# Kernel tuning notes

Hardware: AMD Instinct MI355X
Metric: run time of the kernel (lower is better)

## Reference

```python
import jax, jax.numpy as jnp
import numpy as np

B, T = 256, 2048
K_LABELS = 50
K2 = K_LABELS + 2  # includes START (K) and STOP (K+1) tags
NEG_INF = -10000.0


def setup_inputs() -> dict:
    key = jax.random.key(0)
    k1, k2, k3, k4 = jax.random.split(key, 4)
    emissions = jax.random.normal(k1, (B, T, K2), dtype=jnp.float32)
    transitions = jax.random.normal(k2, (K2, K2), dtype=jnp.float32)
    lengths = jax.random.randint(k3, (B,), 1, T + 1, dtype=jnp.int64)
    labels = jax.random.randint(k4, (B, T), 0, K_LABELS, dtype=jnp.int64)
    return {"emissions": emissions, "transitions": transitions,
            "lengths": lengths, "labels": labels}


def _forward_algo(emissions, transitions, lengths):
    b, t, k2 = emissions.shape
    start_tag, stop_tag = k2 - 2, k2 - 1
    init = jnp.full((k2,), NEG_INF, emissions.dtype).at[start_tag].set(0.0)
    alpha0 = jnp.broadcast_to(init, (b, k2))  # [B, K2]

    def step(alpha, emit):
        # tag_var[b, next, prev] = emit[b, next] + trans[next, prev] + alpha[b, prev]
        tag_var = emit[:, :, None] + transitions[None, :, :] + alpha[:, None, :]
        new_alpha = jax.nn.logsumexp(tag_var, axis=2)  # [B, K2]
        return new_alpha, new_alpha

    _, alphas = jax.lax.scan(step, alpha0, jnp.swapaxes(emissions, 0, 1))
    all_alphas = jnp.concatenate([alpha0[None], alphas], axis=0)  # [T+1, B, K2]
    fv = all_alphas[lengths, jnp.arange(b)]  # alpha at each sequence's final step
    terminal = fv + transitions[stop_tag][None, :]
    return jax.nn.logsumexp(terminal, axis=1)  # [B]


def _score_label(emissions, transitions, lengths, labels):
    b, t, k2 = emissions.shape
    start_tag, stop_tag = k2 - 2, k2 - 1
    start_col = jnp.full((b, 1), start_tag, labels.dtype)
    stop_col = jnp.full((b, 1), stop_tag, labels.dtype)
    pad_start = jnp.concatenate([start_col, labels], axis=1)  # [B, T+1]
    pad_stop = jnp.concatenate([labels, stop_col], axis=1)    # [B, T+1]
    pos = jnp.arange(t + 1)
    pad_stop = jnp.where(pos[None, :] >= lengths[:, None], stop_tag, pad_stop)
    # transition score over positions 0..length (inclusive)
    trans_mask = pos[None, :] <= lengths[:, None]
    trans_sc = jnp.where(trans_mask, transitions[pad_stop, pad_start], 0.0).sum(axis=1)
    # emission score over positions 0..length-1
    emit_mask = jnp.arange(t)[None, :] < lengths[:, None]
    emit_vals = jnp.take_along_axis(emissions, labels[..., None], axis=-1)[..., 0]
    emit_sc = jnp.where(emit_mask, emit_vals, 0.0).sum(axis=1)
    return trans_sc + emit_sc  # [B]


def reference(emissions, transitions, lengths, labels):
    forward_score = _forward_algo(emissions, transitions, lengths)
    gold_score = _score_label(emissions, transitions, lengths, labels)
    return jnp.mean(forward_score - gold_score)
```

## Files before the change

### kernel.cpp

```cpp
#include <hip/hip_runtime.h>


#define B_    256
#define T_    2048
#define K2_   52
#define LOG2E_ 1.4426950408889634f
#define LN2_   0.6931471805599453f

__device__ __forceinline__ int imin(int a, int b) { return a < b ? a : b; }
__device__ __forceinline__ int imax(int a, int b) { return a > b ? a : b; }

#define X2F(e) __builtin_amdgcn_exp2f((e) * LOG2E_)

#define FORALL52(F) \
  F(0) F(1) F(2) F(3) F(4) F(5) F(6) F(7) F(8) F(9) F(10) F(11) F(12) F(13) \
  F(14) F(15) F(16) F(17) F(18) F(19) F(20) F(21) F(22) F(23) F(24) F(25) \
  F(26) F(27) F(28) F(29) F(30) F(31) F(32) F(33) F(34) F(35) F(36) F(37) \
  F(38) F(39) F(40) F(41) F(42) F(43) F(44) F(45) F(46) F(47) F(48) F(49) \
  F(50) F(51)

#define FORALL52C(F) \
  F(0,0) F(1,1) F(2,2) F(3,3) F(4,4) F(5,5) F(6,6) F(7,7) \
  F(8,0) F(9,1) F(10,2) F(11,3) F(12,4) F(13,5) F(14,6) F(15,7) \
  F(16,0) F(17,1) F(18,2) F(19,3) F(20,4) F(21,5) F(22,6) F(23,7) \
  F(24,0) F(25,1) F(26,2) F(27,3) F(28,4) F(29,5) F(30,6) F(31,7) \
  F(32,0) F(33,1) F(34,2) F(35,3) F(36,4) F(37,5) F(38,6) F(39,7) \
  F(40,0) F(41,1) F(42,2) F(43,3) F(44,4) F(45,5) F(46,6) F(47,7) \
  F(48,0) F(49,1) F(50,2) F(51,3)

#define DECLMF(i) float MF_##i; { float _t = tr[n * K2_ + i] * LOG2E_; \
  asm volatile("v_exp_f32 %0, %1\n\ts_nop 1" : "=v"(MF_##i) : "v"(_t)); }
#define DECLMB(i) float MB_##i; { float _t = tr[i * K2_ + n] * LOG2E_; \
  asm volatile("v_exp_f32 %0, %1\n\ts_nop 1" : "=v"(MB_##i) : "v"(_t)); }

#define DECLB(i,c) \
  float _b##i = __int_as_float(__builtin_amdgcn_ds_bpermute(4 * (i), _srci));

#define ACCF(i,c) _a##c = fmaf(MF_##i, _b##i, _a##c);
#define ACCB(i,c) _a##c = fmaf(MB_##i, _b##i, _a##c);

#define MATVEC_F(SRC, OUTY) \
    int _srci = __float_as_int(SRC); \
    FORALL52C(DECLB) \
    float _a0=0.f,_a1=0.f,_a2=0.f,_a3=0.f,_a4=0.f,_a5=0.f,_a6=0.f,_a7=0.f; \
    FORALL52C(ACCF) \
    float OUTY = ((_a0+_a1)+(_a2+_a3)) + ((_a4+_a5)+(_a6+_a7));

#define MATVEC_B(SRC, OUTY) \
    int _srci = __float_as_int(SRC); \
    FORALL52C(DECLB) \
    float _a0=0.f,_a1=0.f,_a2=0.f,_a3=0.f,_a4=0.f,_a5=0.f,_a6=0.f,_a7=0.f; \
    FORALL52C(ACCB) \
    float OUTY = ((_a0+_a1)+(_a2+_a3)) + ((_a4+_a5)+(_a6+_a7));

#define FSTEP_R(EV, NEWIDX) do {                                \
    float _ne = emb[(size_t)(NEWIDX) * K2_ + n];                \
    MATVEC_F(vv, _y)                                            \
    float _m   = _b50;                                          \
    float _inv = __builtin_amdgcn_rcpf(_m);                     \
    C += __builtin_amdgcn_logf(_m);                             \
    vv = _y * (_inv * X2F(EV));                                 \
    EV = _ne;                                                   \
  } while (0)
#define FSTEP_N(EV, NEWIDX) do {                                \
    float _ne = emb[(size_t)(NEWIDX) * K2_ + n];                \
    MATVEC_F(vv, _y)                                            \
    vv = _y * X2F(EV);                                          \
    EV = _ne;                                                   \
  } while (0)

#define BSTEP_R(EV, NEWIDX) do {                                \
    float _ne = emb[(size_t)(NEWIDX) * K2_ + n];                \
    MATVEC_B(vv, _y)                                            \
    float _m   = _b0;                                           \
    float _inv = __builtin_amdgcn_rcpf(_m);                     \
    C += __builtin_amdgcn_logf(_m);                             \
    ub = _y * _inv;                                             \
    vv = ub * X2F(EV);                                          \
    EV = _ne;                                                   \
  } while (0)
#define BSTEP_N(EV, NEWIDX) do {                                \
    float _ne = emb[(size_t)(NEWIDX) * K2_ + n];                \
    MATVEC_B(vv, _y)                                            \
    ub = _y;                                                    \
    vv = ub * X2F(EV);                                          \
    EV = _ne;                                                   \
  } while (0)

__global__ __launch_bounds__(128)
__attribute__((amdgpu_waves_per_eu(1, 1)))
void crf_fwd_kernel(const float* __restrict__ em,
                    const float* __restrict__ tr,
                    const int*  __restrict__ len,
                    const int*  __restrict__ lab,
                    float* __restrict__ per_b)
{
  const int b    = blockIdx.x;
  const int tid  = threadIdx.x;
  const int wave = tid >> 6;
  const int lane = tid & 63;
  const int n    = (lane < K2_) ? lane : (K2_ - 1);
  const int L    = len[b];
  const int h    = L >> 1;
  const float* emb = em + (size_t)b * (T_ * K2_);

  __shared__ float sU[64];
  __shared__ float sCb[1];
  __shared__ float sG[2];

  float vv, C = 0.0f;

  if (wave == 0) {
    FORALL52(DECLMF)
    vv = (lane == 50) ? 1.0f : 0.0f;
    float e0 = emb[0 * K2_ + n];
    float e1 = emb[1 * K2_ + n];
    float e2 = emb[2 * K2_ + n];
    float e3 = emb[3 * K2_ + n];
    int t = 0;
    for (; t + 4 <= h; t += 4) {
      int i4 = imin(t + 4, T_ - 1), i5 = imin(t + 5, T_ - 1);
      int i6 = imin(t + 6, T_ - 1), i7 = imin(t + 7, T_ - 1);
      FSTEP_R(e0, i4);
      FSTEP_N(e1, i5);
      FSTEP_N(e2, i6);
      FSTEP_N(e3, i7);
    }
    int rem = h - t;
    if (rem > 0) FSTEP_R(e0, T_ - 1);
    if (rem > 1) FSTEP_N(e1, T_ - 1);
    if (rem > 2) FSTEP_N(e2, T_ - 1);
  } else {
    FORALL52(DECLMB)
    float ub = X2F(tr[(K2_ - 1) * K2_ + n]);
    int cnt = L - h;
    float e0 = emb[(size_t)(L - 1) * K2_ + n];
    float eA = emb[(size_t)imax(L - 2, 0) * K2_ + n];
    float eB = emb[(size_t)imax(L - 3, 0) * K2_ + n];
    float eC = emb[(size_t)imax(L - 4, 0) * K2_ + n];
    float eD = emb[(size_t)imax(L - 5, 0) * K2_ + n];
    vv = ub * X2F(e0);
    int s = 0;
    for (; s + 4 <= cnt; s += 4) {
      int j4 = imax(L - 6 - s, 0), j5 = imax(L - 7 - s, 0);
      int j6 = imax(L - 8 - s, 0), j7 = imax(L - 9 - s, 0);
      BSTEP_R(eA, j4);
      BSTEP_N(eB, j5);
      BSTEP_N(eC, j6);
      BSTEP_N(eD, j7);
    }
    int rem = cnt - s;
    if (rem > 0) BSTEP_R(eA, 0);
    if (rem > 1) BSTEP_N(eB, 0);
    if (rem > 2) BSTEP_N(eC, 0);

    sU[lane] = ub;
    if (lane == 0) sCb[0] = C;
  }

  float gold = 0.0f;
  const int* labb = lab + b * T_;
  for (int tt = tid; tt < L; tt += 128) {
    int l1 = labb[tt];
    int l0 = (tt == 0) ? 50 : labb[tt - 1];
    gold += emb[(size_t)tt * K2_ + l1] + tr[l1 * K2_ + l0];
  }
  if (tid == 0) gold += tr[(K2_ - 1) * K2_ + labb[L - 1]];
#pragma unroll
  for (int off = 32; off >= 1; off >>= 1)
    gold += __shfl_xor(gold, off, 64);
  if (lane == 0) sG[wave] = gold;

  __syncthreads();

  if (wave == 0) {
    float x = (lane < K2_) ? vv * sU[lane] : 0.0f;
#pragma unroll
    for (int off = 32; off >= 1; off >>= 1)
      x += __shfl_xor(x, off, 64);
    float fwd = (C + sCb[0] + __builtin_amdgcn_logf(x)) * LN2_;
    if (lane == 0) per_b[b] = fwd - (sG[0] + sG[1]);
  }
}

__global__ void reduce_mean_kernel(const float* __restrict__ per_b,
                                   float* __restrict__ out)
{
  const int tid = threadIdx.x;
  float v = per_b[tid];
#pragma unroll
  for (int off = 32; off >= 1; off >>= 1) v += __shfl_xor(v, off, 64);
  __shared__ float s[4];
  if ((tid & 63) == 0) s[tid >> 6] = v;
  __syncthreads();
  if (tid == 0) out[0] = ((s[0] + s[1]) + (s[2] + s[3])) * (1.0f / (float)B_);
}

extern "C" void kernel_launch(void* const* d_in, const int* in_sizes, int n_in,
                              void* d_out, int out_size, void* d_ws, size_t ws_size,
                              hipStream_t stream) {
  const float* em  = (const float*)d_in[0];
  const float* tr  = (const float*)d_in[1];
  const int*   len = (const int*)d_in[2];
  const int*   lab = (const int*)d_in[3];
  float* out = (float*)d_out;
  float* ws  = (float*)d_ws;

  crf_fwd_kernel<<<B_, 128, 0, stream>>>(em, tr, len, lab, ws);
  reduce_mean_kernel<<<1, 256, 0, stream>>>(ws, out);
}
```

Before: 462.1 us.

## Replace bpermute broadcast matvec with DPP row-rotation diagonal matvec

The per-step 52x52 matvec no longer uses 52 ds_bpermute LDS-crossbar ops per step. It stores the exponentiated transition matrix in a diagonal-shifted layout of 64 diagonals per lane and rotates the state vector with a DPP wave-rotate, using two half-wave streams offset by a shfl_xor of 32. The rescale factor now comes from readlane and is hoisted ahead of the matvec. This trades LDS-permute latency for 64 DPP ops plus FMAs per step, with 12 padded diagonals, and adds a runtime check of the rotate direction.

```diff
diff --git a/kernel.cpp b/kernel.cpp
--- a/kernel.cpp
+++ b/kernel.cpp
@@ -9,81 +9,91 @@
 
 __device__ __forceinline__ int imin(int a, int b) { return a < b ? a : b; }
 __device__ __forceinline__ int imax(int a, int b) { return a > b ? a : b; }
+__device__ __forceinline__ float rdlane(float v, int src) {
+  return __uint_as_float(__builtin_amdgcn_readlane(__float_as_uint(v), src));
+}
+__device__ __forceinline__ float rotf(float x) {
+  return __int_as_float(__builtin_amdgcn_update_dpp(
+      __float_as_int(x), __float_as_int(x), 0x13C, 0xF, 0xF, false));
+}
 
 #define X2F(e) __builtin_amdgcn_exp2f((e) * LOG2E_)
 
-#define FORALL52(F) \
+#define FORALL64(F) \
   F(0) F(1) F(2) F(3) F(4) F(5) F(6) F(7) F(8) F(9) F(10) F(11) F(12) F(13) \
   F(14) F(15) F(16) F(17) F(18) F(19) F(20) F(21) F(22) F(23) F(24) F(25) \
   F(26) F(27) F(28) F(29) F(30) F(31) F(32) F(33) F(34) F(35) F(36) F(37) \
   F(38) F(39) F(40) F(41) F(42) F(43) F(44) F(45) F(46) F(47) F(48) F(49) \
-  F(50) F(51)
-
-#define FORALL52C(F) \
-  F(0,0) F(1,1) F(2,2) F(3,3) F(4,4) F(5,5) F(6,6) F(7,7) \
-  F(8,0) F(9,1) F(10,2) F(11,3) F(12,4) F(13,5) F(14,6) F(15,7) \
-  F(16,0) F(17,1) F(18,2) F(19,3) F(20,4) F(21,5) F(22,6) F(23,7) \
-  F(24,0) F(25,1) F(26,2) F(27,3) F(28,4) F(29,5) F(30,6) F(31,7) \
-  F(32,0) F(33,1) F(34,2) F(35,3) F(36,4) F(37,5) F(38,6) F(39,7) \
-  F(40,0) F(41,1) F(42,2) F(43,3) F(44,4) F(45,5) F(46,6) F(47,7) \
-  F(48,0) F(49,1) F(50,2) F(51,3)
-
-#define DECLMF(i) float MF_##i; { float _t = tr[n * K2_ + i] * LOG2E_; \
-  asm volatile("v_exp_f32 %0, %1\n\ts_nop 1" : "=v"(MF_##i) : "v"(_t)); }
-#define DECLMB(i) float MB_##i; { float _t = tr[i * K2_ + n] * LOG2E_; \
-  asm volatile("v_exp_f32 %0, %1\n\ts_nop 1" : "=v"(MB_##i) : "v"(_t)); }
-
-#define DECLB(i,c) \
-  float _b##i = __int_as_float(__builtin_amdgcn_ds_bpermute(4 * (i), _srci));
-
-#define ACCF(i,c) _a##c = fmaf(MF_##i, _b##i, _a##c);
-#define ACCB(i,c) _a##c = fmaf(MB_##i, _b##i, _a##c);
-
-#define MATVEC_F(SRC, OUTY) \
-    int _srci = __float_as_int(SRC); \
-    FORALL52C(DECLB) \
+  F(50) F(51) F(52) F(53) F(54) F(55) F(56) F(57) F(58) F(59) F(60) F(61) \
+  F(62) F(63)
+
+#define DECLDG_F(r) float DG_##r; { \
+  int _col = (lane + ddir * (r)) & 63; \
+  int _cc  = imin(_col, K2_ - 1); \
+  float _t = (lane < K2_ && _col < K2_) ? tr[n * K2_ + _cc] * LOG2E_ : -1.0e30f; \
+  asm volatile("v_exp_f32 %0, %1\n\ts_nop 1" : "=v"(DG_##r) : "v"(_t)); }
+#define DECLDG_B(r) float DG_##r; { \
+  int _col = (lane + ddir * (r)) & 63; \
+  int _cc  = imin(_col, K2_ - 1); \
+  float _t = (lane < K2_ && _col < K2_) ? tr[_cc * K2_ + n] * LOG2E_ : -1.0e30f; \
+  asm volatile("v_exp_f32 %0, %1\n\ts_nop 1" : "=v"(DG_##r) : "v"(_t)); }
+
+#define MVP(k, k32, cA, cB) \
+  _a##cA = fmaf(DG_##k,   _rA, _a##cA);  _rA = rotf(_rA); \
+  _a##cB = fmaf(DG_##k32, _rB, _a##cB);  _rB = rotf(_rB);
+
+#define FOR32P(F) \
+  F(0,32,0,4)  F(1,33,1,5)  F(2,34,2,6)  F(3,35,3,7) \
+  F(4,36,0,4)  F(5,37,1,5)  F(6,38,2,6)  F(7,39,3,7) \
+  F(8,40,0,4)  F(9,41,1,5)  F(10,42,2,6) F(11,43,3,7) \
+  F(12,44,0,4) F(13,45,1,5) F(14,46,2,6) F(15,47,3,7) \
+  F(16,48,0,4) F(17,49,1,5) F(18,50,2,6) F(19,51,3,7) \
+  F(20,52,0,4) F(21,53,1,5) F(22,54,2,6) F(23,55,3,7) \
+  F(24,56,0,4) F(25,57,1,5) F(26,58,2,6) F(27,59,3,7) \
+  F(28,60,0,4) F(29,61,1,5) F(30,62,2,6) F(31,63,3,7)
+
+#define MATVEC64(SRC, SRC32, OUTY) \
+    float _rA = (SRC); \
+    float _rB = (SRC32); \
     float _a0=0.f,_a1=0.f,_a2=0.f,_a3=0.f,_a4=0.f,_a5=0.f,_a6=0.f,_a7=0.f; \
-    FORALL52C(ACCF) \
+    FOR32P(MVP) \
     float OUTY = ((_a0+_a1)+(_a2+_a3)) + ((_a4+_a5)+(_a6+_a7));
 
-#define MATVEC_B(SRC, OUTY) \
-    int _srci = __float_as_int(SRC); \
-    FORALL52C(DECLB) \
-    float _a0=0.f,_a1=0.f,_a2=0.f,_a3=0.f,_a4=0.f,_a5=0.f,_a6=0.f,_a7=0.f; \
-    FORALL52C(ACCB) \
-    float OUTY = ((_a0+_a1)+(_a2+_a3)) + ((_a4+_a5)+(_a6+_a7));
-
 #define FSTEP_R(EV, NEWIDX) do {                                \
     float _ne = emb[(size_t)(NEWIDX) * K2_ + n];                \
-    MATVEC_F(vv, _y)                                            \
-    float _m   = _b50;                                          \
+    float _m  = rdlane(vv, 50);                                 \
     float _inv = __builtin_amdgcn_rcpf(_m);                     \
     C += __builtin_amdgcn_logf(_m);                             \
+    MATVEC64(vv, vx, _y)                                        \
     vv = _y * (_inv * X2F(EV));                                 \
+    vx = __shfl_xor(vv, 32, 64);                                \
     EV = _ne;                                                   \
   } while (0)
 #define FSTEP_N(EV, NEWIDX) do {                                \
     float _ne = emb[(size_t)(NEWIDX) * K2_ + n];                \
-    MATVEC_F(vv, _y)                                            \
+    MATVEC64(vv, vx, _y)                                        \
     vv = _y * X2F(EV);                                          \
+    vx = __shfl_xor(vv, 32, 64);                                \
     EV = _ne;                                                   \
   } while (0)
 
 #define BSTEP_R(EV, NEWIDX) do {                                \
     float _ne = emb[(size_t)(NEWIDX) * K2_ + n];                \
-    MATVEC_B(vv, _y)                                            \
-    float _m   = _b0;                                           \
+    float _m  = rdlane(vv, 0);                                  \
     float _inv = __builtin_amdgcn_rcpf(_m);                     \
     C += __builtin_amdgcn_logf(_m);                             \
+    MATVEC64(vv, vx, _y)                                        \
     ub = _y * _inv;                                             \
     vv = ub * X2F(EV);                                          \
+    vx = __shfl_xor(vv, 32, 64);                                \
     EV = _ne;                                                   \
   } while (0)
 #define BSTEP_N(EV, NEWIDX) do {                                \
     float _ne = emb[(size_t)(NEWIDX) * K2_ + n];                \
-    MATVEC_B(vv, _y)                                            \
+    MATVEC64(vv, vx, _y)                                        \
     ub = _y;                                                    \
     vv = ub * X2F(EV);                                          \
+    vx = __shfl_xor(vv, 32, 64);                                \
     EV = _ne;                                                   \
   } while (0)
 
@@ -108,11 +118,15 @@
   __shared__ float sCb[1];
   __shared__ float sG[2];
 
-  float vv, C = 0.0f;
+  int _pv = __builtin_amdgcn_update_dpp(lane, lane, 0x13C, 0xF, 0xF, false);
+  const int ddir = (__builtin_amdgcn_readlane(_pv, 0) == 1) ? 1 : 63;
+
+  float vv, vx, C = 0.0f;
 
   if (wave == 0) {
-    FORALL52(DECLMF)
+    FORALL64(DECLDG_F)
     vv = (lane == 50) ? 1.0f : 0.0f;
+    vx = __shfl_xor(vv, 32, 64);
     float e0 = emb[0 * K2_ + n];
     float e1 = emb[1 * K2_ + n];
     float e2 = emb[2 * K2_ + n];
@@ -131,8 +145,8 @@
     if (rem > 1) FSTEP_N(e1, T_ - 1);
     if (rem > 2) FSTEP_N(e2, T_ - 1);
   } else {
-    FORALL52(DECLMB)
-    float ub = X2F(tr[(K2_ - 1) * K2_ + n]);
+    FORALL64(DECLDG_B)
+    float ub = (lane < K2_) ? X2F(tr[(K2_ - 1) * K2_ + n]) : 0.0f;
     int cnt = L - h;
     float e0 = emb[(size_t)(L - 1) * K2_ + n];
     float eA = emb[(size_t)imax(L - 2, 0) * K2_ + n];
@@ -140,6 +154,7 @@
     float eC = emb[(size_t)imax(L - 4, 0) * K2_ + n];
     float eD = emb[(size_t)imax(L - 5, 0) * K2_ + n];
     vv = ub * X2F(e0);
+    vx = __shfl_xor(vv, 32, 64);
     int s = 0;
     for (; s + 4 <= cnt; s += 4) {
       int j4 = imax(L - 6 - s, 0), j5 = imax(L - 7 - s, 0);
```

Result: slower. 507.7 us (+9.9%).
